# Performance work log

Measured on AMD Instinct MI355X. Metric: run time of the kernel, lower is better.

The kernel has to match this reference:

```python
import jax, jax.numpy as jnp
import numpy as np

B, S, D_MODEL, H = 4, 1024, 1024, 16
DEPTH = D_MODEL // H


def head_scales():
    # np.arange(0.1, 10 + 0.01, 9.9 / (H - 1)) -> exactly H values from 0.1 to 10.0
    return jnp.asarray(np.arange(0.1, 10 + 0.01, 9.9 / (H - 1)), dtype=jnp.float32)


def setup_inputs() -> dict:
    key = jax.random.key(0)
    ks = jax.random.split(key, 14)
    sd = 1.0 / np.sqrt(D_MODEL)
    inp = {
        "v": jax.random.normal(ks[0], (B, S, D_MODEL), jnp.float32),
        "k": jax.random.normal(ks[1], (B, S, D_MODEL), jnp.float32),
        "q": jax.random.normal(ks[2], (B, S, D_MODEL), jnp.float32),
        # pairwise distance-like weights in [0, 1)
        "weight": jax.random.uniform(ks[3], (B, S, S), jnp.float32),
        # binary padding mask, broadcastable to (B, H, S, S); 1 = masked
        "mask": (jax.random.uniform(ks[4], (B, 1, 1, S)) < 0.1).astype(jnp.float32),
        "Wq": jax.random.normal(ks[5], (D_MODEL, D_MODEL), jnp.float32) * sd,
        "bq": jnp.zeros((D_MODEL,), jnp.float32),
        "Wk": jax.random.normal(ks[6], (D_MODEL, D_MODEL), jnp.float32) * sd,
        "bk": jnp.zeros((D_MODEL,), jnp.float32),
        "Wv": jax.random.normal(ks[7], (D_MODEL, D_MODEL), jnp.float32) * sd,
        "bv": jnp.zeros((D_MODEL,), jnp.float32),
        "Wo": jax.random.normal(ks[8], (D_MODEL, D_MODEL), jnp.float32) * sd,
        "bo": jnp.zeros((D_MODEL,), jnp.float32),
    }
    return inp


def reference(v, k, q, weight, mask, Wq, bq, Wk, bk, Wv, bv, Wo, bo):
    def split_heads(x):  # (B, S, D) -> (B, H, S, depth)
        return x.reshape(B, -1, H, DEPTH).transpose(0, 2, 1, 3)

    qh = split_heads(q @ Wq + bq)
    kh = split_heads(k @ Wk + bk)
    vh = split_heads(v @ Wv + bv)

    # shift_distance[b,h,i,j] = weight[b,i,j] * scale[h]
    scales = head_scales()  # (H,)
    bias = weight[:, None, :, :] * scales[None, :, None, None]  # (B, H, S, S)

    logits = jnp.einsum("bhqd,bhkd->bhqk", qh, kh) / jnp.sqrt(
        jnp.asarray(DEPTH, jnp.float32)
    )
    logits = logits + bias + mask * (-1e9)
    attn = jax.nn.softmax(logits, axis=-1)  # (B, H, S, S)
    out = jnp.einsum("bhqk,bhkd->bhqd", attn, vh)  # (B, H, S, depth)
    out = out.transpose(0, 2, 1, 3).reshape(B, -1, D_MODEL)
    return out @ Wo + bo
```

## Files before the change

### kernel.cpp

```cpp
#include <hip/hip_runtime.h>
#include <hip/hip_fp16.h>

#define DEV __device__ __forceinline__

typedef _Float16 f16x8 __attribute__((ext_vector_type(8)));
typedef _Float16 f16x4 __attribute__((ext_vector_type(4)));
typedef float f32x4 __attribute__((ext_vector_type(4)));

DEV void gload16(void* lds, const void* g) {
  __builtin_amdgcn_global_load_lds((__attribute__((address_space(1))) const void*)g,
                                   (__attribute__((address_space(3))) void*)lds,
                                   16, 0, 0);
}

DEV f32x4 mfma16(f16x8 a, f16x8 b, f32x4 c) {
  return __builtin_amdgcn_mfma_f32_16x16x32_f16(a, b, c, 0, 0, 0);
}

DEV f16x8 cvt8(float4 a, float4 b) {
  f16x8 o;
  o[0] = (_Float16)a.x; o[1] = (_Float16)a.y; o[2] = (_Float16)a.z; o[3] = (_Float16)a.w;
  o[4] = (_Float16)b.x; o[5] = (_Float16)b.y; o[6] = (_Float16)b.z; o[7] = (_Float16)b.w;
  return o;
}

__global__ __launch_bounds__(256) void prep_kernel(
    const float* __restrict__ W0, const float* __restrict__ W1,
    const float* __restrict__ W2, const float* __restrict__ W3,
    const float* __restrict__ weight, const float* __restrict__ q,
    const float* __restrict__ k, const float* __restrict__ v,
    _Float16* __restrict__ Wt, _Float16* __restrict__ Wh,
    _Float16* __restrict__ Ah) {
  __shared__ float tile[32][33];
  const int i = blockIdx.x;
  if (i < 4096) {
    const int z = i >> 10, bb = i & 1023;
    const float* W = (z == 0) ? W0 : (z == 1) ? W1 : (z == 2) ? W2 : W3;
    _Float16* dst = Wt + (size_t)z * (1024 * 1024);
    const int tx = threadIdx.x & 31, ty = threadIdx.x >> 5;
    const int n0 = (bb & 31) * 32, k0 = (bb >> 5) * 32;
#pragma unroll
    for (int r = 0; r < 4; ++r)
      tile[ty + r * 8][tx] = W[(size_t)(k0 + ty + r * 8) * 1024 + n0 + tx];
    __syncthreads();
#pragma unroll
    for (int r = 0; r < 4; ++r)
      dst[(size_t)(n0 + ty + r * 8) * 1024 + k0 + tx] = (_Float16)tile[tx][ty + r * 8];
  } else if (i < 6144) {
    const size_t j = (size_t)(i - 4096) * 256 + threadIdx.x;
    float4 a = *(const float4*)(weight + j * 8);
    float4 b = *(const float4*)(weight + j * 8 + 4);
    *(f16x8*)(Wh + j * 8) = cvt8(a, b);
  } else {
    const int j = i - 6144;
    const int y = j >> 11, x = j & 2047;
    const float* src = (y == 0) ? q : (y == 1) ? k : v;
    _Float16* dst = Ah + (size_t)y * (4096ull * 1024);
    const size_t idx = ((size_t)x * 256 + threadIdx.x) * 8;
    float4 a = *(const float4*)(src + idx);
    float4 b = *(const float4*)(src + idx + 4);
    *(f16x8*)(dst + idx) = cvt8(a, b);
  }
}

template <int BM, bool AF32>
DEV void gemm_core(const void* __restrict__ Aptr, const _Float16* __restrict__ Bt,
                   _Float16* Al, _Float16* Bl, int m0, int n0,
                   f32x4 (&acc)[4][4]) {
  constexpr int AS = AF32 ? 40 : 32;
  constexpr int WR = BM / 64, WC = 4 / WR, NI = (128 / WC) / 16;
  const int t = threadIdx.x;
  const int l = t & 63, w = t >> 6;
  const int wr = w / WC, wc = w % WC;
  const int lo = l & 15, lg = l >> 4;

  for (int ks = 0; ks < 1024; ks += 32) {
    __syncthreads();
    gload16(&Bl[t * 8], Bt + (size_t)(n0 + (t >> 2)) * 1024 + ks + (t & 3) * 8);
    gload16(&Bl[(t + 256) * 8], Bt + (size_t)(n0 + (t >> 2) + 64) * 1024 + ks + (t & 3) * 8);
    if constexpr (AF32) {
      const float* Ag = (const float*)Aptr;
      const int row = t >> 1, c0 = (t & 1) * 16;
      const float4* src = (const float4*)(Ag + (size_t)(m0 + row) * 1024 + ks + c0);
      float4 f0 = src[0], f1 = src[1], f2 = src[2], f3 = src[3];
      *(f16x8*)&Al[row * AS + c0] = cvt8(f0, f1);
      *(f16x8*)&Al[row * AS + c0 + 8] = cvt8(f2, f3);
    } else {
      const _Float16* Ag = (const _Float16*)Aptr;
      gload16(&Al[t * 8], Ag + (size_t)(m0 + (t >> 2)) * 1024 + ks + (t & 3) * 8);
      if constexpr (BM == 128)
        gload16(&Al[(t + 256) * 8], Ag + (size_t)(m0 + (t >> 2) + 64) * 1024 + ks + (t & 3) * 8);
    }
    __syncthreads();

    f16x8 af[4], bf[NI];
#pragma unroll
    for (int mi = 0; mi < 4; ++mi)
      af[mi] = *(const f16x8*)&Al[(wr * 64 + mi * 16 + lo) * AS + lg * 8];
#pragma unroll
    for (int ni = 0; ni < NI; ++ni)
      bf[ni] = *(const f16x8*)&Bl[(wc * (NI * 16) + ni * 16 + lo) * 32 + lg * 8];
#pragma unroll
    for (int mi = 0; mi < 4; ++mi)
#pragma unroll
      for (int ni = 0; ni < NI; ++ni)
        acc[mi][ni] = mfma16(af[mi], bf[ni], acc[mi][ni]);
  }
}

template <bool AHALF>
__global__ __launch_bounds__(256) void proj_kernel(
    const _Float16* __restrict__ Ah, const float* __restrict__ qin,
    const float* __restrict__ kin, const float* __restrict__ vin,
    const _Float16* __restrict__ Wt, const float* __restrict__ bq,
    const float* __restrict__ bk, const float* __restrict__ bv,
    _Float16* __restrict__ Qh, _Float16* __restrict__ Kt,
    _Float16* __restrict__ Vt) {
  __shared__ __attribute__((aligned(16))) _Float16 Al[128 * 40];
  __shared__ __attribute__((aligned(16))) _Float16 Bl[128 * 32];
  const int lin = blockIdx.x + (blockIdx.y << 3) + (blockIdx.z << 8);
  const int work = (lin & 7) * 96 + (lin >> 3);
  const int z = work >> 8;
  const int m0 = ((work & 255) >> 3) * 128;
  const int n0 = (work & 7) * 128;

  const _Float16* Bt = Wt + (size_t)z * (1 << 20);
  const float* bias = (z == 0) ? bq : (z == 1) ? bk : bv;
  _Float16* C = (z == 0) ? Qh : (z == 1) ? Kt : Vt;

  f32x4 acc[4][4];
#pragma unroll
  for (int i = 0; i < 4; ++i)
#pragma unroll
    for (int j = 0; j < 4; ++j) acc[i][j] = (f32x4){0.f, 0.f, 0.f, 0.f};
  if constexpr (AHALF) {
    gemm_core<128, false>(Ah + (size_t)z * (4096ull * 1024), Bt, Al, Bl, m0, n0, acc);
  } else {
    const float* A = (z == 0) ? qin : (z == 1) ? kin : vin;
    gemm_core<128, true>(A, Bt, Al, Bl, m0, n0, acc);
  }

  const int l = threadIdx.x & 63, w = threadIdx.x >> 6;
  const int wr = w >> 1, wc = w & 1;
  const int lo = l & 15, lg = l >> 4;
#pragma unroll
  for (int mi = 0; mi < 4; ++mi) {
#pragma unroll
    for (int ni = 0; ni < 4; ++ni) {
      const int col = n0 + wc * 64 + ni * 16 + lo;
      const int rowb = m0 + wr * 64 + mi * 16 + lg * 4;
      const float bc = bias[col];
      const int h = col >> 6, d = col & 63;
#pragma unroll
      for (int r = 0; r < 4; ++r) {
        const float vv = acc[mi][ni][r] + bc;
        const int m = rowb + r;
        const int b = m >> 10, s = m & 1023;
        const size_t slab = (size_t)(b * 16 + h) * 65536;
        if (z == 0) {
          C[slab + (size_t)s * 64 + d] = (_Float16)vv;
        } else if (z == 1) {
          C[slab + (size_t)(s >> 6) * 4096 + (size_t)(s & 63) * 64 +
            (((d >> 3) ^ (s & 7)) << 3) + (d & 7)] = (_Float16)vv;
        } else {
          C[slab + (size_t)(s >> 6) * 4096 + (size_t)d * 64 +
            ((((s >> 3) & 7) ^ (d & 7)) << 3) + (s & 7)] = (_Float16)vv;
        }
      }
    }
  }
}

__global__ __launch_bounds__(256) void outproj_kernel(
    const _Float16* __restrict__ AO, const _Float16* __restrict__ Bt,
    const float* __restrict__ bias, float* __restrict__ out) {
  __shared__ __attribute__((aligned(16))) _Float16 Al[64 * 32];
  __shared__ __attribute__((aligned(16))) _Float16 Bl[128 * 32];
  const int lin = blockIdx.x + (blockIdx.y << 3);
  const int work = (lin & 7) * 64 + (lin >> 3);
  const int m0 = (work >> 3) * 64;
  const int n0 = (work & 7) * 128;
  f32x4 acc[4][4];
#pragma unroll
  for (int i = 0; i < 4; ++i)
#pragma unroll
    for (int j = 0; j < 4; ++j) acc[i][j] = (f32x4){0.f, 0.f, 0.f, 0.f};
  gemm_core<64, false>(AO, Bt, Al, Bl, m0, n0, acc);

  const int l = threadIdx.x & 63, w = threadIdx.x >> 6;
  const int wc = w;
  const int lo = l & 15, lg = l >> 4;
#pragma unroll
  for (int mi = 0; mi < 4; ++mi) {
#pragma unroll
    for (int ni = 0; ni < 2; ++ni) {
      const int col = n0 + wc * 32 + ni * 16 + lo;
      const int rowb = m0 + mi * 16 + lg * 4;
      const float bc = bias[col];
#pragma unroll
      for (int r = 0; r < 4; ++r)
        out[(size_t)(rowb + r) * 1024 + col] = acc[mi][ni][r] + bc;
    }
  }
}

template <int NSPLIT>
__global__ __launch_bounds__(512, 4) void attn_kernel(
    const _Float16* __restrict__ Qh, const _Float16* __restrict__ Kt,
    const _Float16* __restrict__ Vt, const _Float16* __restrict__ Wh,
    const float* __restrict__ mask, void* __restrict__ Oout,
    float2* __restrict__ Sst) {
  __shared__ __attribute__((aligned(16))) _Float16 Kl[2][4096];
  __shared__ __attribute__((aligned(16))) _Float16 Vl[2][4096];
  __shared__ __attribute__((aligned(16))) _Float16 Pl[8][16][72];
  const int t = threadIdx.x, l = t & 63, w = t >> 6;
  const int lo = l & 15, lg = l >> 4;
  const int bh = blockIdx.y, b = bh >> 4, h = bh & 15;
  const int q0w = blockIdx.x * 128 + w * 16;
  const int sp = (NSPLIT > 1) ? blockIdx.z : 0;
  constexpr int NKT = 16 / NSPLIT;
  const int kt0 = sp * NKT;
  constexpr float L2E = 1.44269504089f;
  const float scale = 0.1f + (float)h * (9.9f / 15.0f);
  const float cS = 0.125f * L2E;
  const float cW = scale * L2E;
  const float cM = -1e9f * L2E;
  const _Float16* Kslab = Kt + (size_t)bh * 65536;
  const _Float16* Vslab = Vt + (size_t)bh * 65536;
  const _Float16* Wb = Wh + ((size_t)b << 20);
  const float* Mb = mask + (size_t)b * 1024;
  const int qrow = q0w + lg * 4;
  const int sl = lg ^ (lo & 7);

  const f16x8 qf0 = *(const f16x8*)(Qh + (size_t)bh * 65536 + (q0w + lo) * 64 + lg * 8);
  const f16x8 qf1 = *(const f16x8*)(Qh + (size_t)bh * 65536 + (q0w + lo) * 64 + 32 + lg * 8);

  f32x4 oacc[4];
#pragma unroll
  for (int di = 0; di < 4; ++di) oacc[di] = (f32x4){0.f, 0.f, 0.f, 0.f};
  float mrun[4], lsum[4];
#pragma unroll
  for (int r = 0; r < 4; ++r) { mrun[r] = -1e38f; lsum[r] = 0.f; }

  gload16(&Kl[0][t * 8], Kslab + (size_t)kt0 * 4096 + t * 8);
  gload16(&Vl[0][t * 8], Vslab + (size_t)kt0 * 4096 + t * 8);
  __syncthreads();

  for (int it = 0; it < NKT; ++it) {
    const int kt = kt0 + it;
    const int cur = it & 1;
    if (it + 1 < NKT) {
      gload16(&Kl[cur ^ 1][t * 8], Kslab + (size_t)(kt + 1) * 4096 + t * 8);
      gload16(&Vl[cur ^ 1][t * 8], Vslab + (size_t)(kt + 1) * 4096 + t * 8);
    }
    const int kv0 = kt * 64;
    const _Float16* Kb = Kl[cur];
    const _Float16* Vb = Vl[cur];

    float sv[4][4];
    float tm[4] = {-1e38f, -1e38f, -1e38f, -1e38f};
#pragma unroll
    for (int ni = 0; ni < 4; ++ni) {
      const int key = kv0 + ni * 16 + lo;
      const float mkv = Mb[key] * cM;
      float wgt[4];
#pragma unroll
      for (int r = 0; r < 4; ++r)
        wgt[r] = (float)Wb[(size_t)(qrow + r) * 1024 + key];
      const int kr = ni * 16 + lo;
      f16x8 kf0 = *(const f16x8*)(Kb + kr * 64 + sl * 8);
      f16x8 kf1 = *(const f16x8*)(Kb + kr * 64 + (sl ^ 4) * 8);
      f32x4 s = (f32x4){0.f, 0.f, 0.f, 0.f};
      s = mfma16(qf0, kf0, s);
      s = mfma16(qf1, kf1, s);
#pragma unroll
      for (int r = 0; r < 4; ++r) {
        const float x = s[r] * cS + wgt[r] * cW + mkv;
        sv[ni][r] = x;
        tm[r] = fmaxf(tm[r], x);
      }
    }
#pragma unroll
    for (int st = 1; st < 16; st <<= 1)
#pragma unroll
      for (int r = 0; r < 4; ++r) tm[r] = fmaxf(tm[r], __shfl_xor(tm[r], st));
    float delta = tm[0] - mrun[0];
#pragma unroll
    for (int r = 1; r < 4; ++r) delta = fmaxf(delta, tm[r] - mrun[r]);
    if (!__all(delta <= 8.0f)) {
      float fr[4];
#pragma unroll
      for (int r = 0; r < 4; ++r) {
        const float mn = fmaxf(mrun[r], tm[r]);
        fr[r] = exp2f(mrun[r] - mn);
        mrun[r] = mn;
        lsum[r] *= fr[r];
      }
#pragma unroll
      for (int di = 0; di < 4; ++di)
#pragma unroll
        for (int r = 0; r < 4; ++r) oacc[di][r] *= fr[r];
    }
#pragma unroll
    for (int ni = 0; ni < 4; ++ni)
#pragma unroll
      for (int r = 0; r < 4; ++r) {
        const float p = exp2f(sv[ni][r] - mrun[r]);
        lsum[r] += p;
        Pl[w][lg * 4 + r][ni * 16 + lo] = (_Float16)p;
      }
    const f16x8 pa0 = *(const f16x8*)(&Pl[w][lo][lg * 8]);
    const f16x8 pa1 = *(const f16x8*)(&Pl[w][lo][32 + lg * 8]);
    __builtin_amdgcn_s_setprio(1);
#pragma unroll
    for (int di = 0; di < 4; ++di) {
      const int d = di * 16 + lo;
      f16x8 vf0 = *(const f16x8*)(Vb + d * 64 + sl * 8);
      f16x8 vf1 = *(const f16x8*)(Vb + d * 64 + (sl ^ 4) * 8);
      oacc[di] = mfma16(pa0, vf0, oacc[di]);
      oacc[di] = mfma16(pa1, vf1, oacc[di]);
    }
    __builtin_amdgcn_s_setprio(0);
    __syncthreads();
  }

#pragma unroll
  for (int st = 1; st < 16; st <<= 1)
#pragma unroll
    for (int r = 0; r < 4; ++r) lsum[r] += __shfl_xor(lsum[r], st);

  if constexpr (NSPLIT > 1) {
    if (lo == 0) {
#pragma unroll
      for (int r = 0; r < 4; ++r)
        Sst[(size_t)sp * 65536 + bh * 1024 + qrow + r] = make_float2(mrun[r], lsum[r]);
    }
    _Float16* Op = (_Float16*)Oout + (size_t)sp * (64ull * 1024 * 64);
#pragma unroll
    for (int r = 0; r < 4; ++r) {
      const float inv = 1.0f / lsum[r];
#pragma unroll
      for (int di = 0; di < 4; ++di)
        Op[((size_t)bh * 1024 + qrow + r) * 64 + di * 16 + lo] =
            (_Float16)(oacc[di][r] * inv);
    }
  } else {
    _Float16* AO = (_Float16*)Oout;
#pragma unroll
    for (int r = 0; r < 4; ++r) {
      const float inv = 1.0f / lsum[r];
#pragma unroll
      for (int di = 0; di < 4; ++di)
        AO[((size_t)(b * 1024) + qrow + r) * 1024 + h * 64 + di * 16 + lo] =
            (_Float16)(oacc[di][r] * inv);
    }
  }
}

__global__ __launch_bounds__(256) void merge_kernel(
    const _Float16* __restrict__ Op, const float2* __restrict__ Sst,
    _Float16* __restrict__ AO) {
  const int idx = blockIdx.x * 256 + threadIdx.x;
  const int dc = idx & 15;
  const int qq = (idx >> 4) & 1023;
  const int bh = idx >> 14;
  const int b = bh >> 4, h = bh & 15;
  const float2 s1 = Sst[bh * 1024 + qq];
  const float2 s2 = Sst[65536 + bh * 1024 + qq];
  const float m = fmaxf(s1.x, s2.x);
  float w1 = exp2f(s1.x - m) * s1.y;
  float w2 = exp2f(s2.x - m) * s2.y;
  const float inv = 1.f / (w1 + w2);
  w1 *= inv; w2 *= inv;
  const size_t o = ((size_t)bh * 1024 + qq) * 64 + dc * 4;
  const f16x4 o1 = *(const f16x4*)(Op + o);
  const f16x4 o2 = *(const f16x4*)(Op + (64ull * 1024 * 64) + o);
  f16x4 r;
#pragma unroll
  for (int j = 0; j < 4; ++j)
    r[j] = (_Float16)(w1 * (float)o1[j] + w2 * (float)o2[j]);
  *(f16x4*)(AO + ((size_t)(b * 1024 + qq) * 1024 + h * 64 + dc * 4)) = r;
}

extern "C" void kernel_launch(void* const* d_in, const int* in_sizes, int n_in,
                              void* d_out, int out_size, void* d_ws, size_t ws_size,
                              hipStream_t stream) {
  (void)in_sizes; (void)n_in; (void)out_size;
  const float* v      = (const float*)d_in[0];
  const float* k      = (const float*)d_in[1];
  const float* q      = (const float*)d_in[2];
  const float* weight = (const float*)d_in[3];
  const float* mask   = (const float*)d_in[4];
  const float* Wq = (const float*)d_in[5];
  const float* bq = (const float*)d_in[6];
  const float* Wk = (const float*)d_in[7];
  const float* bk = (const float*)d_in[8];
  const float* Wv = (const float*)d_in[9];
  const float* bv = (const float*)d_in[10];
  const float* Wo = (const float*)d_in[11];
  const float* bo = (const float*)d_in[12];
  float* out = (float*)d_out;

  const size_t MB = 1ull << 20;
  char* ws = (char*)d_ws;
  _Float16* Wt = (_Float16*)ws;
  _Float16* Qh = (_Float16*)(ws + 8 * MB);
  _Float16* Kt = (_Float16*)(ws + 16 * MB);
  _Float16* Vt = (_Float16*)(ws + 24 * MB);
  _Float16* Wh = (_Float16*)(ws + 32 * MB);
  _Float16* Ah = (_Float16*)(ws + 40 * MB);
  _Float16* Op = (_Float16*)(ws + 40 * MB);
  float2*  Sst = (float2*)(ws + 56 * MB);
  _Float16* AO = Qh;

  if (ws_size >= 64 * MB) {
    prep_kernel<<<12288, 256, 0, stream>>>(Wq, Wk, Wv, Wo, weight, q, k, v, Wt, Wh, Ah);
    proj_kernel<true><<<dim3(8, 32, 3), 256, 0, stream>>>(Ah, q, k, v, Wt, bq, bk, bv,
                                                          Qh, Kt, Vt);
    attn_kernel<2><<<dim3(8, 64, 2), 512, 0, stream>>>(Qh, Kt, Vt, Wh, mask, Op, Sst);
    merge_kernel<<<4096, 256, 0, stream>>>(Op, Sst, AO);
    outproj_kernel<<<dim3(8, 64), 256, 0, stream>>>(AO, Wt + 3 * (1 << 20), bo, out);
  } else {
    prep_kernel<<<6144, 256, 0, stream>>>(Wq, Wk, Wv, Wo, weight, q, k, v, Wt, Wh, Ah);
    _Float16* AO2 = (_Float16*)(ws + 40 * MB);
    proj_kernel<false><<<dim3(8, 32, 3), 256, 0, stream>>>(nullptr, q, k, v, Wt, bq, bk,
                                                           bv, Qh, Kt, Vt);
    attn_kernel<1><<<dim3(8, 64, 1), 512, 0, stream>>>(Qh, Kt, Vt, Wh, mask, AO2, nullptr);
    outproj_kernel<<<dim3(8, 64), 256, 0, stream>>>(AO2, Wt + 3 * (1 << 20), bo, out);
  }
}
```

Measured before the change: 147.9 us.

## Shrink attention key tile to 32 with V tile loaded every other step

Halves the key tile processed per loop iteration from 64 to 32 keys. K is now staged in 32-key slabs, and the K layout written by the projection kernel changes to a flat per-row swizzle. V is still loaded in 64-key slabs, once every two iterations, with the swizzle selecting the correct half. This cuts per-iteration register use (score array, P buffer) and LDS footprint, which may allow more overlap. The cost is twice as many barriers and online-softmax rescale checks per key.

Measured after the change: 172.8 us. +16.9%, slower.

```diff
diff --git a/kernel.cpp b/kernel.cpp
--- a/kernel.cpp
+++ b/kernel.cpp
@@ -160,7 +160,7 @@
         if (z == 0) {
           C[slab + (size_t)s * 64 + d] = (_Float16)vv;
         } else if (z == 1) {
-          C[slab + (size_t)(s >> 6) * 4096 + (size_t)(s & 63) * 64 +
+          C[slab + (size_t)s * 64 +
             (((d >> 3) ^ (s & 7)) << 3) + (d & 7)] = (_Float16)vv;
         } else {
           C[slab + (size_t)(s >> 6) * 4096 + (size_t)d * 64 +
@@ -210,15 +210,15 @@
     const _Float16* __restrict__ Vt, const _Float16* __restrict__ Wh,
     const float* __restrict__ mask, void* __restrict__ Oout,
     float2* __restrict__ Sst) {
-  __shared__ __attribute__((aligned(16))) _Float16 Kl[2][4096];
+  __shared__ __attribute__((aligned(16))) _Float16 Kl[2][2048];
   __shared__ __attribute__((aligned(16))) _Float16 Vl[2][4096];
-  __shared__ __attribute__((aligned(16))) _Float16 Pl[8][16][72];
+  __shared__ __attribute__((aligned(16))) _Float16 Pl[8][16][40];
   const int t = threadIdx.x, l = t & 63, w = t >> 6;
   const int lo = l & 15, lg = l >> 4;
   const int bh = blockIdx.y, b = bh >> 4, h = bh & 15;
   const int q0w = blockIdx.x * 128 + w * 16;
   const int sp = (NSPLIT > 1) ? blockIdx.z : 0;
-  constexpr int NKT = 16 / NSPLIT;
+  constexpr int NKT = 32 / NSPLIT;
   const int kt0 = sp * NKT;
   constexpr float L2E = 1.44269504089f;
   const float scale = 0.1f + (float)h * (9.9f / 15.0f);
@@ -242,25 +242,25 @@
 #pragma unroll
   for (int r = 0; r < 4; ++r) { mrun[r] = -1e38f; lsum[r] = 0.f; }
 
-  gload16(&Kl[0][t * 8], Kslab + (size_t)kt0 * 4096 + t * 8);
-  gload16(&Vl[0][t * 8], Vslab + (size_t)kt0 * 4096 + t * 8);
+  if (t < 256) gload16(&Kl[0][t * 8], Kslab + (size_t)kt0 * 2048 + t * 8);
+  gload16(&Vl[0][t * 8], Vslab + (size_t)(kt0 >> 1) * 4096 + t * 8);
   __syncthreads();
 
   for (int it = 0; it < NKT; ++it) {
     const int kt = kt0 + it;
-    const int cur = it & 1;
-    if (it + 1 < NKT) {
-      gload16(&Kl[cur ^ 1][t * 8], Kslab + (size_t)(kt + 1) * 4096 + t * 8);
-      gload16(&Vl[cur ^ 1][t * 8], Vslab + (size_t)(kt + 1) * 4096 + t * 8);
-    }
-    const int kv0 = kt * 64;
-    const _Float16* Kb = Kl[cur];
-    const _Float16* Vb = Vl[cur];
-
-    float sv[4][4];
+    if (it + 1 < NKT && t < 256)
+      gload16(&Kl[(it + 1) & 1][t * 8], Kslab + (size_t)(kt + 1) * 2048 + t * 8);
+    if ((it & 1) == 0 && it + 2 < NKT)
+      gload16(&Vl[((it >> 1) + 1) & 1][t * 8],
+              Vslab + (size_t)((kt >> 1) + 1) * 4096 + t * 8);
+    const int kv0 = kt * 32;
+    const _Float16* Kb = Kl[it & 1];
+    const _Float16* Vb = Vl[(it >> 1) & 1];
+
+    float sv[2][4];
     float tm[4] = {-1e38f, -1e38f, -1e38f, -1e38f};
 #pragma unroll
-    for (int ni = 0; ni < 4; ++ni) {
+    for (int ni = 0; ni < 2; ++ni) {
       const int key = kv0 + ni * 16 + lo;
       const float mkv = Mb[key] * cM;
       float wgt[4];
@@ -302,23 +302,21 @@
         for (int r = 0; r < 4; ++r) oacc[di][r] *= fr[r];
     }
 #pragma unroll
-    for (int ni = 0; ni < 4; ++ni)
+    for (int ni = 0; ni < 2; ++ni)
 #pragma unroll
       for (int r = 0; r < 4; ++r) {
         const float p = exp2f(sv[ni][r] - mrun[r]);
         lsum[r] += p;
         Pl[w][lg * 4 + r][ni * 16 + lo] = (_Float16)p;
       }
-    const f16x8 pa0 = *(const f16x8*)(&Pl[w][lo][lg * 8]);
-    const f16x8 pa1 = *(const f16x8*)(&Pl[w][lo][32 + lg * 8]);
+    const f16x8 pa = *(const f16x8*)(&Pl[w][lo][lg * 8]);
+    const int vsl = sl ^ ((it & 1) << 2);
     __builtin_amdgcn_s_setprio(1);
 #pragma unroll
     for (int di = 0; di < 4; ++di) {
       const int d = di * 16 + lo;
-      f16x8 vf0 = *(const f16x8*)(Vb + d * 64 + sl * 8);
-      f16x8 vf1 = *(const f16x8*)(Vb + d * 64 + (sl ^ 4) * 8);
-      oacc[di] = mfma16(pa0, vf0, oacc[di]);
-      oacc[di] = mfma16(pa1, vf1, oacc[di]);
+      f16x8 vf = *(const f16x8*)(Vb + d * 64 + vsl * 8);
+      oacc[di] = mfma16(pa, vf, oacc[di]);
     }
     __builtin_amdgcn_s_setprio(0);
     __syncthreads();
```

## Drop split-KV attention and merge pass; use 64-row tiles for QKV projection

Applied to the files above, without the earlier changes.

Attention now always processes all 16 KV tiles in one workgroup and writes the normalized output straight into the head-interleaved activation buffer. This removes the partial-output and stats writes, the separate merge kernel and its launch. The QKV projection on the large-workspace path is templated on tile height and launched with 64-row tiles, doubling the number of workgroups, with the work-order swizzle generalized to match. The cost is half as many attention workgroups, each running a longer serial KV loop, on a GPU with many CUs.

Result: no change. 150.8 us (+2.0%).

```diff
diff --git a/kernel.cpp b/kernel.cpp
--- a/kernel.cpp
+++ b/kernel.cpp
@@ -71,7 +71,8 @@
   constexpr int WR = BM / 64, WC = 4 / WR, NI = (128 / WC) / 16;
   const int t = threadIdx.x;
   const int l = t & 63, w = t >> 6;
-  const int wr = w / WC, wc = w % WC;
+  const int wr = (WR == 2) ? (w >> 1) : 0;
+  const int wc = (WR == 2) ? (w & 1) : w;
   const int lo = l & 15, lg = l >> 4;
 
   for (int ks = 0; ks < 1024; ks += 32) {
@@ -108,7 +109,7 @@
   }
 }
 
-template <bool AHALF>
+template <int BM, bool AHALF>
 __global__ __launch_bounds__(256) void proj_kernel(
     const _Float16* __restrict__ Ah, const float* __restrict__ qin,
     const float* __restrict__ kin, const float* __restrict__ vin,
@@ -116,13 +117,16 @@
     const float* __restrict__ bk, const float* __restrict__ bv,
     _Float16* __restrict__ Qh, _Float16* __restrict__ Kt,
     _Float16* __restrict__ Vt) {
-  __shared__ __attribute__((aligned(16))) _Float16 Al[128 * 40];
+  __shared__ __attribute__((aligned(16))) _Float16 Al[BM * 40];
   __shared__ __attribute__((aligned(16))) _Float16 Bl[128 * 32];
-  const int lin = blockIdx.x + (blockIdx.y << 3) + (blockIdx.z << 8);
-  const int work = (lin & 7) * 96 + (lin >> 3);
-  const int z = work >> 8;
-  const int m0 = ((work & 255) >> 3) * 128;
-  const int n0 = (work & 7) * 128;
+  constexpr int NWG_Z = (4096 / BM) * 8;
+  constexpr int CHUNK = (3 * NWG_Z) / 8;
+  const int lin = blockIdx.x + (blockIdx.y << 3) + blockIdx.z * NWG_Z;
+  const int work = (lin & 7) * CHUNK + (lin >> 3);
+  const int z = work / NWG_Z;
+  const int rem = work % NWG_Z;
+  const int m0 = (rem >> 3) * BM;
+  const int n0 = (rem & 7) * 128;
 
   const _Float16* Bt = Wt + (size_t)z * (1 << 20);
   const float* bias = (z == 0) ? bq : (z == 1) ? bk : bv;
@@ -134,20 +138,22 @@
 #pragma unroll
     for (int j = 0; j < 4; ++j) acc[i][j] = (f32x4){0.f, 0.f, 0.f, 0.f};
   if constexpr (AHALF) {
-    gemm_core<128, false>(Ah + (size_t)z * (4096ull * 1024), Bt, Al, Bl, m0, n0, acc);
+    gemm_core<BM, false>(Ah + (size_t)z * (4096ull * 1024), Bt, Al, Bl, m0, n0, acc);
   } else {
     const float* A = (z == 0) ? qin : (z == 1) ? kin : vin;
-    gemm_core<128, true>(A, Bt, Al, Bl, m0, n0, acc);
-  }
-
+    gemm_core<BM, true>(A, Bt, Al, Bl, m0, n0, acc);
+  }
+
+  constexpr int WR = BM / 64, WC = 4 / WR, NI = (128 / WC) / 16;
   const int l = threadIdx.x & 63, w = threadIdx.x >> 6;
-  const int wr = w >> 1, wc = w & 1;
+  const int wr = (WR == 2) ? (w >> 1) : 0;
+  const int wc = (WR == 2) ? (w & 1) : w;
   const int lo = l & 15, lg = l >> 4;
 #pragma unroll
   for (int mi = 0; mi < 4; ++mi) {
 #pragma unroll
-    for (int ni = 0; ni < 4; ++ni) {
-      const int col = n0 + wc * 64 + ni * 16 + lo;
+    for (int ni = 0; ni < NI; ++ni) {
+      const int col = n0 + wc * (NI * 16) + ni * 16 + lo;
       const int rowb = m0 + wr * 64 + mi * 16 + lg * 4;
       const float bc = bias[col];
       const int h = col >> 6, d = col & 63;
@@ -204,12 +210,10 @@
   }
 }
 
-template <int NSPLIT>
 __global__ __launch_bounds__(512, 4) void attn_kernel(
     const _Float16* __restrict__ Qh, const _Float16* __restrict__ Kt,
     const _Float16* __restrict__ Vt, const _Float16* __restrict__ Wh,
-    const float* __restrict__ mask, void* __restrict__ Oout,
-    float2* __restrict__ Sst) {
+    const float* __restrict__ mask, _Float16* __restrict__ AO) {
   __shared__ __attribute__((aligned(16))) _Float16 Kl[2][4096];
   __shared__ __attribute__((aligned(16))) _Float16 Vl[2][4096];
   __shared__ __attribute__((aligned(16))) _Float16 Pl[8][16][72];
@@ -217,9 +221,6 @@
   const int lo = l & 15, lg = l >> 4;
   const int bh = blockIdx.y, b = bh >> 4, h = bh & 15;
   const int q0w = blockIdx.x * 128 + w * 16;
-  const int sp = (NSPLIT > 1) ? blockIdx.z : 0;
-  constexpr int NKT = 16 / NSPLIT;
-  const int kt0 = sp * NKT;
   constexpr float L2E = 1.44269504089f;
   const float scale = 0.1f + (float)h * (9.9f / 15.0f);
   const float cS = 0.125f * L2E;
@@ -242,18 +243,17 @@
 #pragma unroll
   for (int r = 0; r < 4; ++r) { mrun[r] = -1e38f; lsum[r] = 0.f; }
 
-  gload16(&Kl[0][t * 8], Kslab + (size_t)kt0 * 4096 + t * 8);
-  gload16(&Vl[0][t * 8], Vslab + (size_t)kt0 * 4096 + t * 8);
+  gload16(&Kl[0][t * 8], Kslab + t * 8);
+  gload16(&Vl[0][t * 8], Vslab + t * 8);
   __syncthreads();
 
-  for (int it = 0; it < NKT; ++it) {
-    const int kt = kt0 + it;
+  for (int it = 0; it < 16; ++it) {
     const int cur = it & 1;
-    if (it + 1 < NKT) {
-      gload16(&Kl[cur ^ 1][t * 8], Kslab + (size_t)(kt + 1) * 4096 + t * 8);
-      gload16(&Vl[cur ^ 1][t * 8], Vslab + (size_t)(kt + 1) * 4096 + t * 8);
-    }
-    const int kv0 = kt * 64;
+    if (it + 1 < 16) {
+      gload16(&Kl[cur ^ 1][t * 8], Kslab + (size_t)(it + 1) * 4096 + t * 8);
+      gload16(&Vl[cur ^ 1][t * 8], Vslab + (size_t)(it + 1) * 4096 + t * 8);
+    }
+    const int kv0 = it * 64;
     const _Float16* Kb = Kl[cur];
     const _Float16* Vb = Vl[cur];
 
@@ -329,57 +329,14 @@
 #pragma unroll
     for (int r = 0; r < 4; ++r) lsum[r] += __shfl_xor(lsum[r], st);
 
-  if constexpr (NSPLIT > 1) {
-    if (lo == 0) {
-#pragma unroll
-      for (int r = 0; r < 4; ++r)
-        Sst[(size_t)sp * 65536 + bh * 1024 + qrow + r] = make_float2(mrun[r], lsum[r]);
-    }
-    _Float16* Op = (_Float16*)Oout + (size_t)sp * (64ull * 1024 * 64);
-#pragma unroll
-    for (int r = 0; r < 4; ++r) {
-      const float inv = 1.0f / lsum[r];
-#pragma unroll
-      for (int di = 0; di < 4; ++di)
-        Op[((size_t)bh * 1024 + qrow + r) * 64 + di * 16 + lo] =
-            (_Float16)(oacc[di][r] * inv);
-    }
-  } else {
-    _Float16* AO = (_Float16*)Oout;
-#pragma unroll
-    for (int r = 0; r < 4; ++r) {
-      const float inv = 1.0f / lsum[r];
-#pragma unroll
-      for (int di = 0; di < 4; ++di)
-        AO[((size_t)(b * 1024) + qrow + r) * 1024 + h * 64 + di * 16 + lo] =
-            (_Float16)(oacc[di][r] * inv);
-    }
-  }
-}
-
-__global__ __launch_bounds__(256) void merge_kernel(
-    const _Float16* __restrict__ Op, const float2* __restrict__ Sst,
-    _Float16* __restrict__ AO) {
-  const int idx = blockIdx.x * 256 + threadIdx.x;
-  const int dc = idx & 15;
-  const int qq = (idx >> 4) & 1023;
-  const int bh = idx >> 14;
-  const int b = bh >> 4, h = bh & 15;
-  const float2 s1 = Sst[bh * 1024 + qq];
-  const float2 s2 = Sst[65536 + bh * 1024 + qq];
-  const float m = fmaxf(s1.x, s2.x);
-  float w1 = exp2f(s1.x - m) * s1.y;
-  float w2 = exp2f(s2.x - m) * s2.y;
-  const float inv = 1.f / (w1 + w2);
-  w1 *= inv; w2 *= inv;
-  const size_t o = ((size_t)bh * 1024 + qq) * 64 + dc * 4;
-  const f16x4 o1 = *(const f16x4*)(Op + o);
-  const f16x4 o2 = *(const f16x4*)(Op + (64ull * 1024 * 64) + o);
-  f16x4 r;
-#pragma unroll
-  for (int j = 0; j < 4; ++j)
-    r[j] = (_Float16)(w1 * (float)o1[j] + w2 * (float)o2[j]);
-  *(f16x4*)(AO + ((size_t)(b * 1024 + qq) * 1024 + h * 64 + dc * 4)) = r;
+#pragma unroll
+  for (int r = 0; r < 4; ++r) {
+    const float inv = 1.0f / lsum[r];
+#pragma unroll
+    for (int di = 0; di < 4; ++di)
+      AO[((size_t)(b * 1024) + qrow + r) * 1024 + h * 64 + di * 16 + lo] =
+          (_Float16)(oacc[di][r] * inv);
+  }
 }
 
 extern "C" void kernel_launch(void* const* d_in, const int* in_sizes, int n_in,
@@ -409,23 +366,17 @@
   _Float16* Vt = (_Float16*)(ws + 24 * MB);
   _Float16* Wh = (_Float16*)(ws + 32 * MB);
   _Float16* Ah = (_Float16*)(ws + 40 * MB);
-  _Float16* Op = (_Float16*)(ws + 40 * MB);
-  float2*  Sst = (float2*)(ws + 56 * MB);
-  _Float16* AO = Qh;
+  _Float16* AO = (_Float16*)(ws + 40 * MB);
 
   if (ws_size >= 64 * MB) {
     prep_kernel<<<12288, 256, 0, stream>>>(Wq, Wk, Wv, Wo, weight, q, k, v, Wt, Wh, Ah);
-    proj_kernel<true><<<dim3(8, 32, 3), 256, 0, stream>>>(Ah, q, k, v, Wt, bq, bk, bv,
-                                                          Qh, Kt, Vt);
-    attn_kernel<2><<<dim3(8, 64, 2), 512, 0, stream>>>(Qh, Kt, Vt, Wh, mask, Op, Sst);
-    merge_kernel<<<4096, 256, 0, stream>>>(Op, Sst, AO);
-    outproj_kernel<<<dim3(8, 64), 256, 0, stream>>>(AO, Wt + 3 * (1 << 20), bo, out);
+    proj_kernel<64, true><<<dim3(8, 64, 3), 256, 0, stream>>>(Ah, q, k, v, Wt, bq, bk,
+                                                              bv, Qh, Kt, Vt);
   } else {
     prep_kernel<<<6144, 256, 0, stream>>>(Wq, Wk, Wv, Wo, weight, q, k, v, Wt, Wh, Ah);
-    _Float16* AO2 = (_Float16*)(ws + 40 * MB);
-    proj_kernel<false><<<dim3(8, 32, 3), 256, 0, stream>>>(nullptr, q, k, v, Wt, bq, bk,
-                                                           bv, Qh, Kt, Vt);
-    attn_kernel<1><<<dim3(8, 64, 1), 512, 0, stream>>>(Qh, Kt, Vt, Wh, mask, AO2, nullptr);
-    outproj_kernel<<<dim3(8, 64), 256, 0, stream>>>(AO2, Wt + 3 * (1 << 20), bo, out);
-  }
-}
+    proj_kernel<128, false><<<dim3(8, 32, 3), 256, 0, stream>>>(nullptr, q, k, v, Wt,
+                                                                bq, bk, bv, Qh, Kt, Vt);
+  }
+  attn_kernel<<<dim3(8, 64), 512, 0, stream>>>(Qh, Kt, Vt, Wh, mask, AO);
+  outproj_kernel<<<dim3(8, 64), 256, 0, stream>>>(AO, Wt + 3 * (1 << 20), bo, out);
+}
```
